# Performance work log

Hardware: AMD Instinct MI355X
Metric: run time of the kernel (lower is better)

## Reference

```python
import jax, jax.numpy as jnp
import numpy as np

B, Q, K, QS, KS, H, DV = 16, 128, 512, 256, 256, 128, 256


def setup_inputs() -> dict:
    key = jax.random.key(0)
    ks = jax.random.split(key, 7)
    return {
        "queries": jax.random.normal(ks[0], (B, Q, QS), dtype=jnp.float32),
        "keys": jax.random.normal(ks[1], (B, K, KS), dtype=jnp.float32),
        "values": jax.random.normal(ks[2], (B, K, DV), dtype=jnp.float32),
        "valid_lens": jax.random.randint(ks[3], (B,), 1, K + 1),
        # Linear weights (no bias); stored as [in, hidden] so x @ W == nn.Linear
        "W_q": jax.random.normal(ks[4], (QS, H), dtype=jnp.float32) / np.float32(np.sqrt(QS)),
        "W_k": jax.random.normal(ks[5], (KS, H), dtype=jnp.float32) / np.float32(np.sqrt(KS)),
        "w_v": jax.random.normal(ks[6], (H,), dtype=jnp.float32) / np.float32(np.sqrt(H)),
    }


def reference(queries, keys, values, valid_lens, W_q, W_k, w_v):
    # Projections
    q = jnp.einsum('bqd,dh->bqh', queries, W_q)   # [B,Q,H]
    k = jnp.einsum('bkd,dh->bkh', keys, W_k)      # [B,K,H]
    # Additive (Bahdanau) score: tanh(q + k) . w_v  -> [B,Q,K]
    feats = jnp.tanh(q[:, :, None, :] + k[:, None, :, :])  # [B,Q,K,H] big intermediate
    scores = jnp.einsum('bqkh,h->bqk', feats, w_v)
    # masked softmax over keys: positions >= valid_len get -1e6 (as in torch ref)
    mask = jnp.arange(K)[None, None, :] < valid_lens[:, None, None]  # [B,1,K] bcast
    scores = jnp.where(mask, scores, jnp.float32(-1e6))
    attn = jax.nn.softmax(scores, axis=-1)        # [B,Q,K]
    # dropout p=0.0 -> identity
    return jnp.einsum('bqk,bkd->bqd', attn, values)  # [B,Q,DV]
```

## Files before the change

kernel.cpp:

```cpp
#include <hip/hip_runtime.h>
#include <hip/hip_bf16.h>

#define NB 16
#define NQ 128
#define NK 512
#define DIN 256
#define NH 128
#define NDV 256

#define CSC 2.8853900817779268f

__global__ __launch_bounds__(256) void proj_both_kernel(
    const float* __restrict__ Q, const float* __restrict__ K,
    const float* __restrict__ Wq, const float* __restrict__ Wk,
    const int* __restrict__ vlen,
    float* __restrict__ EQ, float* __restrict__ EKT)
{
    __shared__ float Xl[32 * DIN];
    __shared__ float Wl[64 * NH];
    const int tid = threadIdx.x;
    int blk = blockIdx.x;
    const float* X; const float* W;
    int b, r0, isq;
    if (blk < 64) { isq = 1; b = blk >> 2; r0 = (blk & 3) * 32;
                    X = Q + ((size_t)b * NQ + r0) * DIN; W = Wq; }
    else { blk -= 64; isq = 0; b = blk >> 4; r0 = (blk & 15) * 32;
           X = K + ((size_t)b * NK + r0) * DIN; W = Wk;
           int vl = vlen[b]; vl = vl < 1 ? 1 : (vl > NK ? NK : vl);
           if (r0 >= vl) return;
    }

    {
        const float4* Xg = (const float4*)X;
        float4* Xs = (float4*)Xl;
        #pragma unroll
        for (int i = 0; i < 8; ++i) Xs[tid + 256 * i] = Xg[tid + 256 * i];
    }

    const int h4 = tid & 31;
    const int rg = tid >> 5;
    const float4* Wg = (const float4*)W;
    float4* Ws4 = (float4*)Wl;

    float4 acc[4];
    #pragma unroll
    for (int r = 0; r < 4; ++r) { acc[r].x = 0.f; acc[r].y = 0.f; acc[r].z = 0.f; acc[r].w = 0.f; }

    float4 pre[8];
    #pragma unroll
    for (int j = 0; j < 8; ++j) pre[j] = Wg[tid + 256 * j];
    #pragma unroll
    for (int j = 0; j < 8; ++j) Ws4[tid + 256 * j] = pre[j];

    for (int c = 0; c < 4; ++c) {
        if (c < 3) {
            #pragma unroll
            for (int j = 0; j < 8; ++j) pre[j] = Wg[(c + 1) * 2048 + tid + 256 * j];
        }
        __syncthreads();

        const float* Xc = &Xl[c * 64];
        #pragma unroll 4
        for (int dd = 0; dd < 64; dd += 4) {
            float4 w0 = *(const float4*)&Wl[(dd + 0) * NH + 4 * h4];
            float4 w1 = *(const float4*)&Wl[(dd + 1) * NH + 4 * h4];
            float4 w2 = *(const float4*)&Wl[(dd + 2) * NH + 4 * h4];
            float4 w3 = *(const float4*)&Wl[(dd + 3) * NH + 4 * h4];
            #pragma unroll
            for (int r = 0; r < 4; ++r) {
                float4 x = *(const float4*)&Xc[(rg * 4 + r) * DIN + dd];
                acc[r].x += x.x * w0.x + x.y * w1.x + x.z * w2.x + x.w * w3.x;
                acc[r].y += x.x * w0.y + x.y * w1.y + x.z * w2.y + x.w * w3.y;
                acc[r].z += x.x * w0.z + x.y * w1.z + x.z * w2.z + x.w * w3.z;
                acc[r].w += x.x * w0.w + x.y * w1.w + x.z * w2.w + x.w * w3.w;
            }
        }
        __syncthreads();
        if (c < 3) {
            #pragma unroll
            for (int j = 0; j < 8; ++j) Ws4[tid + 256 * j] = pre[j];
        }
    }

    #pragma unroll
    for (int r = 0; r < 4; ++r) {
        acc[r].x = __builtin_amdgcn_exp2f(CSC * acc[r].x);
        acc[r].y = __builtin_amdgcn_exp2f(CSC * acc[r].y);
        acc[r].z = __builtin_amdgcn_exp2f(CSC * acc[r].z);
        acc[r].w = __builtin_amdgcn_exp2f(CSC * acc[r].w);
    }

    if (isq) {
        #pragma unroll
        for (int r = 0; r < 4; ++r)
            *(float4*)&EQ[((size_t)b * NQ + r0 + rg * 4 + r) * NH + 4 * h4] = acc[r];
    } else {
        float* T = Xl;
        __syncthreads();
        #pragma unroll
        for (int r = 0; r < 4; ++r) {
            T[(4 * h4 + 0) * 36 + rg * 4 + r] = acc[r].x;
            T[(4 * h4 + 1) * 36 + rg * 4 + r] = acc[r].y;
            T[(4 * h4 + 2) * 36 + rg * 4 + r] = acc[r].z;
            T[(4 * h4 + 3) * 36 + rg * 4 + r] = acc[r].w;
        }
        __syncthreads();
        #pragma unroll
        for (int i = 0; i < 4; ++i) {
            const int idx = tid + 256 * i;
            const int h = idx >> 3, c8 = idx & 7;
            float4 v = *(const float4*)&T[h * 36 + c8 * 4];
            *(float4*)&EKT[((size_t)b * NH + h) * NK + r0 + c8 * 4] = v;
        }
    }
}

__global__ __launch_bounds__(512) void attn_fused_kernel(
    const float* __restrict__ EQ, const float* __restrict__ EKT,
    const float* __restrict__ wv, const int* __restrict__ vlen,
    const float* __restrict__ V, float* __restrict__ OUT)
{
    __shared__ float eq4[NH * 4];
    __shared__ float wvl[NH];
    __shared__ float sc[4][NK];
    __shared__ float part[4][4][NDV];
    const int tid = threadIdx.x;
    const int b  = blockIdx.x & 15;
    const int q0 = (blockIdx.x >> 4) * 4;

    {
        const int r = tid >> 7, h = tid & 127;
        eq4[h * 4 + r] = EQ[((size_t)b * NQ + q0 + r) * NH + h];
    }
    if (tid < NH) wvl[tid] = -2.0f * wv[tid];
    __syncthreads();

    int vl = vlen[b];
    vl = vl < 1 ? 1 : (vl > NK ? NK : vl);

    {
        float a0 = 0.f, a1 = 0.f, a2 = 0.f, a3 = 0.f;
        const bool vld = (tid < vl);
        if (vld) {
            const float* kb = EKT + (size_t)b * NH * NK + tid;
            #pragma unroll 8
            for (int h = 0; h < NH; ++h) {
                float ek = kb[(size_t)h * NK];
                float4 eq = *(const float4*)&eq4[h * 4];
                float wq = wvl[h];
                a0 += wq * __builtin_amdgcn_rcpf(__builtin_fmaf(eq.x, ek, 1.0f));
                a1 += wq * __builtin_amdgcn_rcpf(__builtin_fmaf(eq.y, ek, 1.0f));
                a2 += wq * __builtin_amdgcn_rcpf(__builtin_fmaf(eq.z, ek, 1.0f));
                a3 += wq * __builtin_amdgcn_rcpf(__builtin_fmaf(eq.w, ek, 1.0f));
            }
        }
        sc[0][tid] = vld ? a0 : -1e6f;
        sc[1][tid] = vld ? a1 : -1e6f;
        sc[2][tid] = vld ? a2 : -1e6f;
        sc[3][tid] = vld ? a3 : -1e6f;
    }
    __syncthreads();

    const int w = tid >> 6, lane = tid & 63;
    if (w < 4) {
        float vals[8];
        float m = -3.0e38f;
        #pragma unroll
        for (int i = 0; i < 8; ++i) { vals[i] = sc[w][lane + 64 * i]; m = fmaxf(m, vals[i]); }
        #pragma unroll
        for (int off = 32; off; off >>= 1) m = fmaxf(m, __shfl_xor(m, off, 64));
        float s = 0.f;
        #pragma unroll
        for (int i = 0; i < 8; ++i) {
            vals[i] = __builtin_amdgcn_exp2f((vals[i] - m) * 1.4426950408889634f);
            s += vals[i];
        }
        #pragma unroll
        for (int off = 32; off; off >>= 1) s += __shfl_xor(s, off, 64);
        const float invs = 1.0f / s;
        #pragma unroll
        for (int i = 0; i < 8; ++i) sc[w][lane + 64 * i] = vals[i] * invs;
    }
    __syncthreads();

    float4 o[4];
    #pragma unroll
    for (int r = 0; r < 4; ++r) { o[r].x = 0.f; o[r].y = 0.f; o[r].z = 0.f; o[r].w = 0.f; }
    {
        const int kb0 = w * 64;
        if (kb0 < vl) {
            const float* vb = V + (size_t)b * NK * NDV + lane * 4;
            #pragma unroll 4
            for (int kk = 0; kk < 64; ++kk) {
                const int k = kb0 + kk;
                float4 v4 = *(const float4*)(vb + (size_t)k * NDV);
                float p0 = sc[0][k], p1 = sc[1][k], p2 = sc[2][k], p3 = sc[3][k];
                o[0].x += p0 * v4.x; o[0].y += p0 * v4.y; o[0].z += p0 * v4.z; o[0].w += p0 * v4.w;
                o[1].x += p1 * v4.x; o[1].y += p1 * v4.y; o[1].z += p1 * v4.z; o[1].w += p1 * v4.w;
                o[2].x += p2 * v4.x; o[2].y += p2 * v4.y; o[2].z += p2 * v4.z; o[2].w += p2 * v4.w;
                o[3].x += p3 * v4.x; o[3].y += p3 * v4.y; o[3].z += p3 * v4.z; o[3].w += p3 * v4.w;
            }
        }
    }
    if (w >= 4) {
        #pragma unroll
        for (int r = 0; r < 4; ++r) *(float4*)&part[w - 4][r][lane * 4] = o[r];
    }
    __syncthreads();
    if (w < 4) {
        #pragma unroll
        for (int r = 0; r < 4; ++r) {
            float4 t = *(const float4*)&part[w][r][lane * 4];
            o[r].x += t.x; o[r].y += t.y; o[r].z += t.z; o[r].w += t.w;
            *(float4*)&part[w][r][lane * 4] = o[r];
        }
    }
    __syncthreads();
    if (tid < 256) {
        const int r = tid >> 6, d4 = tid & 63;
        float4 s = {0.f, 0.f, 0.f, 0.f};
        #pragma unroll
        for (int p = 0; p < 4; ++p) {
            float4 q = *(const float4*)&part[p][r][d4 * 4];
            s.x += q.x; s.y += q.y; s.z += q.z; s.w += q.w;
        }
        *(float4*)&OUT[((size_t)b * NQ + q0 + r) * NDV + d4 * 4] = s;
    }
}

extern "C" void kernel_launch(void* const* d_in, const int* in_sizes, int n_in,
                              void* d_out, int out_size, void* d_ws, size_t ws_size,
                              hipStream_t stream) {
    const float* queries = (const float*)d_in[0];
    const float* keys    = (const float*)d_in[1];
    const float* values  = (const float*)d_in[2];
    const int*   vlen    = (const int*)d_in[3];
    const float* Wq      = (const float*)d_in[4];
    const float* Wk      = (const float*)d_in[5];
    const float* wv      = (const float*)d_in[6];
    float* out           = (float*)d_out;

    float* eq  = (float*)d_ws;
    float* ekt = eq + (size_t)NB * NQ * NH;

    proj_both_kernel<<<64 + 256, 256, 0, stream>>>(queries, keys, Wq, Wk, vlen, eq, ekt);
    attn_fused_kernel<<<NB * 32, 512, 0, stream>>>(eq, ekt, wv, vlen, values, out);
}
```

Baseline: 125.4 us.

## Pair reciprocals across heads, interleave score layout, bound PV loop by valid length

The score loop now processes two hidden units at once and merges w0/y0 + w1/y1 into a single reciprocal of y0*y1, halving the transcendental rcp count per score. Scores are stored interleaved as float4 per key, so the PV loop reads all four query probabilities in one LDS load. The PV loop is also bounded by the valid length so masked keys are skipped. The risk is that the product y0*y1 may overflow or lose precision for large arguments, and the interleaved softmax reads are strided in LDS.

```diff
diff --git a/kernel.cpp b/kernel.cpp
--- a/kernel.cpp
+++ b/kernel.cpp
@@ -122,7 +122,7 @@
 {
     __shared__ float eq4[NH * 4];
     __shared__ float wvl[NH];
-    __shared__ float sc[4][NK];
+    __shared__ float sc4[NK * 4];
     __shared__ float part[4][4][NDV];
     const int tid = threadIdx.x;
     const int b  = blockIdx.x & 15;
@@ -143,21 +143,45 @@
         const bool vld = (tid < vl);
         if (vld) {
             const float* kb = EKT + (size_t)b * NH * NK + tid;
-            #pragma unroll 8
-            for (int h = 0; h < NH; ++h) {
-                float ek = kb[(size_t)h * NK];
-                float4 eq = *(const float4*)&eq4[h * 4];
-                float wq = wvl[h];
-                a0 += wq * __builtin_amdgcn_rcpf(__builtin_fmaf(eq.x, ek, 1.0f));
-                a1 += wq * __builtin_amdgcn_rcpf(__builtin_fmaf(eq.y, ek, 1.0f));
-                a2 += wq * __builtin_amdgcn_rcpf(__builtin_fmaf(eq.z, ek, 1.0f));
-                a3 += wq * __builtin_amdgcn_rcpf(__builtin_fmaf(eq.w, ek, 1.0f));
+            #pragma unroll 4
+            for (int h = 0; h < NH; h += 2) {
+                float ek0 = kb[(size_t)h * NK];
+                float ek1 = kb[(size_t)(h + 1) * NK];
+                float4 ea = *(const float4*)&eq4[h * 4];
+                float4 eb = *(const float4*)&eq4[(h + 1) * 4];
+                float w0 = wvl[h], w1 = wvl[h + 1];
+                {
+                    float y0 = __builtin_fmaf(ea.x, ek0, 1.0f);
+                    float y1 = __builtin_fmaf(eb.x, ek1, 1.0f);
+                    float n  = __builtin_fmaf(w0, y1, w1 * y0);
+                    a0 = __builtin_fmaf(n, __builtin_amdgcn_rcpf(y0 * y1), a0);
+                }
+                {
+                    float y0 = __builtin_fmaf(ea.y, ek0, 1.0f);
+                    float y1 = __builtin_fmaf(eb.y, ek1, 1.0f);
+                    float n  = __builtin_fmaf(w0, y1, w1 * y0);
+                    a1 = __builtin_fmaf(n, __builtin_amdgcn_rcpf(y0 * y1), a1);
+                }
+                {
+                    float y0 = __builtin_fmaf(ea.z, ek0, 1.0f);
+                    float y1 = __builtin_fmaf(eb.z, ek1, 1.0f);
+                    float n  = __builtin_fmaf(w0, y1, w1 * y0);
+                    a2 = __builtin_fmaf(n, __builtin_amdgcn_rcpf(y0 * y1), a2);
+                }
+                {
+                    float y0 = __builtin_fmaf(ea.w, ek0, 1.0f);
+                    float y1 = __builtin_fmaf(eb.w, ek1, 1.0f);
+                    float n  = __builtin_fmaf(w0, y1, w1 * y0);
+                    a3 = __builtin_fmaf(n, __builtin_amdgcn_rcpf(y0 * y1), a3);
+                }
             }
         }
-        sc[0][tid] = vld ? a0 : -1e6f;
-        sc[1][tid] = vld ? a1 : -1e6f;
-        sc[2][tid] = vld ? a2 : -1e6f;
-        sc[3][tid] = vld ? a3 : -1e6f;
+        float4 sv;
+        sv.x = vld ? a0 : -1e6f;
+        sv.y = vld ? a1 : -1e6f;
+        sv.z = vld ? a2 : -1e6f;
+        sv.w = vld ? a3 : -1e6f;
+        *(float4*)&sc4[tid * 4] = sv;
     }
     __syncthreads();
 
@@ -166,7 +190,7 @@
         float vals[8];
         float m = -3.0e38f;
         #pragma unroll
-        for (int i = 0; i < 8; ++i) { vals[i] = sc[w][lane + 64 * i]; m = fmaxf(m, vals[i]); }
+        for (int i = 0; i < 8; ++i) { vals[i] = sc4[(lane + 64 * i) * 4 + w]; m = fmaxf(m, vals[i]); }
         #pragma unroll
         for (int off = 32; off; off >>= 1) m = fmaxf(m, __shfl_xor(m, off, 64));
         float s = 0.f;
@@ -179,7 +203,7 @@
         for (int off = 32; off; off >>= 1) s += __shfl_xor(s, off, 64);
         const float invs = 1.0f / s;
         #pragma unroll
-        for (int i = 0; i < 8; ++i) sc[w][lane + 64 * i] = vals[i] * invs;
+        for (int i = 0; i < 8; ++i) sc4[(lane + 64 * i) * 4 + w] = vals[i] * invs;
     }
     __syncthreads();
 
@@ -189,16 +213,17 @@
     {
         const int kb0 = w * 64;
         if (kb0 < vl) {
+            const int kn = (vl - kb0 < 64) ? (vl - kb0) : 64;
             const float* vb = V + (size_t)b * NK * NDV + lane * 4;
-            #pragma unroll 4
-            for (int kk = 0; kk < 64; ++kk) {
+            #pragma unroll 8
+            for (int kk = 0; kk < kn; ++kk) {
                 const int k = kb0 + kk;
                 float4 v4 = *(const float4*)(vb + (size_t)k * NDV);
-                float p0 = sc[0][k], p1 = sc[1][k], p2 = sc[2][k], p3 = sc[3][k];
-                o[0].x += p0 * v4.x; o[0].y += p0 * v4.y; o[0].z += p0 * v4.z; o[0].w += p0 * v4.w;
-                o[1].x += p1 * v4.x; o[1].y += p1 * v4.y; o[1].z += p1 * v4.z; o[1].w += p1 * v4.w;
-                o[2].x += p2 * v4.x; o[2].y += p2 * v4.y; o[2].z += p2 * v4.z; o[2].w += p2 * v4.w;
-                o[3].x += p3 * v4.x; o[3].y += p3 * v4.y; o[3].z += p3 * v4.z; o[3].w += p3 * v4.w;
+                float4 p  = *(const float4*)&sc4[k * 4];
+                o[0].x += p.x * v4.x; o[0].y += p.x * v4.y; o[0].z += p.x * v4.z; o[0].w += p.x * v4.w;
+                o[1].x += p.y * v4.x; o[1].y += p.y * v4.y; o[1].z += p.y * v4.z; o[1].w += p.y * v4.w;
+                o[2].x += p.z * v4.x; o[2].y += p.z * v4.y; o[2].z += p.z * v4.z; o[2].w += p.z * v4.w;
+                o[3].x += p.w * v4.x; o[3].y += p.w * v4.y; o[3].z += p.w * v4.z; o[3].w += p.w * v4.w;
             }
         }
     }
```

New measurement: 125.3 us. About the same (-0.1%).
